# Kernel optimization log

Hardware: AMD Instinct MI355X
Metric: run time of the kernel (lower is better)

Reference implementation:

```python
import jax, jax.numpy as jnp
import numpy as np

N_AGENTS, RNN_H, N_HEADS, GAT_D, EMB, SDIM = 16, 64, 4, 32, 32, 128


def setup_inputs() -> dict:
    key = jax.random.key(0)
    ks = jax.random.split(key, 16)
    xav = lambda k, shp: jax.random.normal(k, shp, jnp.float32) * (2.0 / sum(shp)) ** 0.5
    return {
        'agent_qs': jax.random.normal(ks[0], (32, 128, N_AGENTS), jnp.float32),
        'states': jax.random.normal(ks[1], (32, 128, SDIM), jnp.float32),
        'hidden_states': jax.random.normal(ks[2], (32, 128, N_AGENTS, RNN_H), jnp.float32),
        'uncertainty': jax.random.uniform(ks[3], (32, 128, 1), jnp.float32),
        'W_gat': xav(ks[4], (RNN_H, N_HEADS * GAT_D)) * 1.414,
        'att_a': xav(ks[5], (1, N_HEADS, 2 * GAT_D)) * 1.414,
        'w1s_W': xav(ks[6], (SDIM + 1, N_HEADS * EMB * GAT_D)),
        'w1s_b': jnp.zeros((N_HEADS * EMB * GAT_D,), jnp.float32),
        'b1_W': xav(ks[7], (SDIM, EMB)),
        'b1_b': jnp.zeros((EMB,), jnp.float32),
        'wf_W': xav(ks[8], (SDIM, EMB)),
        'wf_b': jnp.zeros((EMB,), jnp.float32),
        'V1_W': xav(ks[9], (SDIM, EMB)),
        'V1_b': jnp.zeros((EMB,), jnp.float32),
        'V2_W': xav(ks[10], (EMB, 1)),
        'V2_b': jnp.zeros((1,), jnp.float32),
    }


def gat(h, W_gat, att_a):
    B, n, _ = h.shape
    hp = (h @ W_gat).reshape(B, n, N_HEADS, GAT_D).transpose(0, 2, 1, 3)  # (B,H,n,d)
    a_src, a_dst = att_a[0, :, :GAT_D], att_a[0, :, GAT_D:]  # (H,d) each
    # e[b,h,i,j] = <hp_i, a_src> + <hp_j, a_dst>  (same math as concat+dot)
    src = jnp.einsum('bhnd,hd->bhn', hp, a_src)
    dst = jnp.einsum('bhnd,hd->bhn', hp, a_dst)
    e = jax.nn.leaky_relu(src[:, :, :, None] + dst[:, :, None, :], 0.2)
    attn = jax.nn.softmax(e, axis=-1)
    return jax.nn.elu(jnp.einsum('bhij,bhjd->bhid', attn, hp))  # (B,H,n,d)


def reference(agent_qs, states, hidden_states, uncertainty, W_gat, att_a,
              w1s_W, w1s_b, b1_W, b1_b, wf_W, wf_b, V1_W, V1_b, V2_W, V2_b):
    bs = agent_qs.shape[0]
    s = states.reshape(-1, SDIM)                      # (B,S)
    qs = agent_qs.reshape(-1, 1, N_AGENTS)            # (B,1,n)
    hs = hidden_states.reshape(-1, N_AGENTS, RNN_H)   # (B,n,R)
    unc = uncertainty.reshape(-1, 1)
    s_aug = jnp.concatenate([s, unc], axis=1)         # (B,S+1)

    g = gat(hs, W_gat, att_a)                         # (B,H,n,d)

    w1_state = (s_aug @ w1s_W + w1s_b).reshape(-1, N_HEADS, EMB, GAT_D)
    w1_heads = jnp.abs(jnp.einsum('bhed,bhnd->bhen', w1_state, g))  # (B,H,E,n)
    w1 = w1_heads.mean(axis=1).transpose(0, 2, 1)     # (B,n,E)

    b1 = (s @ b1_W + b1_b)[:, None, :]                # (B,1,E)
    hidden = jax.nn.elu(jnp.einsum('bin,bne->bie', qs, w1) + b1)  # (B,1,E)

    w_final = jnp.abs(s @ wf_W + wf_b)[:, :, None]    # (B,E,1)
    v = (jax.nn.relu(s @ V1_W + V1_b) @ V2_W + V2_b)[:, None, :]  # (B,1,1)
    y = jnp.einsum('bie,bej->bij', hidden, w_final) + v
    return y.reshape(bs, -1, 1)
```

## Files before the change

### kernel.cpp

```cpp
#include <hip/hip_runtime.h>
#include <math.h>


typedef __attribute__((ext_vector_type(8))) short short8;
typedef __attribute__((ext_vector_type(8))) unsigned short ushort8;
typedef __attribute__((ext_vector_type(4))) unsigned short ushort4v;
typedef __attribute__((ext_vector_type(4))) float float4v;
typedef __attribute__((ext_vector_type(4))) _Float16 half4v;

static __device__ inline unsigned short f2bf(float f) {
    unsigned int x;
    __builtin_memcpy(&x, &f, 4);
    unsigned int r = x + 0x7fffu + ((x >> 16) & 1u);
    return (unsigned short)(r >> 16);
}

static __device__ inline short8 pack8(float4 f0, float4 f1) {
    ushort8 o;
    o[0] = f2bf(f0.x); o[1] = f2bf(f0.y); o[2] = f2bf(f0.z); o[3] = f2bf(f0.w);
    o[4] = f2bf(f1.x); o[5] = f2bf(f1.y); o[6] = f2bf(f1.z); o[7] = f2bf(f1.w);
    short8 s;
    __builtin_memcpy(&s, &o, 16);
    return s;
}

__global__ __launch_bounds__(256) void k0_prep(
    const float* __restrict__ w1s_W,
    const float* __restrict__ W_gat,
    const float* __restrict__ att_a,
    const float* __restrict__ states,
    const float* __restrict__ b1_W, const float* __restrict__ b1_b,
    const float* __restrict__ wf_W, const float* __restrict__ wf_b,
    const float* __restrict__ V1_W, const float* __restrict__ V1_b,
    const float* __restrict__ V2_W, const float* __restrict__ V2_b,
    unsigned short* __restrict__ w1sTf,
    unsigned short* __restrict__ WgTf,
    float* __restrict__ b1v, float* __restrict__ wfv,
    float* __restrict__ out)
{
    __shared__ __align__(16) char SMEM[49152];
    const int tid = threadIdx.x, bx = blockIdx.x;

    if (bx < 256) {
        unsigned short* T = (unsigned short*)SMEM;
        const int c0 = bx * 16;
        const int cc = tid & 15, kr = tid >> 4;
        #pragma unroll
        for (int t = 0; t < 8; ++t) {
            int k = t * 16 + kr;
            T[cc * 136 + k] = f2bf(w1s_W[(size_t)k * 4096 + c0 + cc]);
        }
        __syncthreads();
        const int ks = tid >> 6, q = (tid >> 4) & 3, mm = tid & 15;
        *(ushort8*)&w1sTf[(size_t)bx * 2048 + tid * 8] =
            *(const ushort8*)&T[mm * 136 + ks * 32 + q * 8];
    } else if (bx == 256) {
        unsigned short* T = (unsigned short*)SMEM;
        #pragma unroll
        for (int t = 0; t < 32; ++t) {
            int i = t * 256 + tid;
            int k = i >> 7, c = i & 127;
            T[c * 72 + k] = f2bf(W_gat[k * 128 + c]);
        }
        __syncthreads();
        #pragma unroll
        for (int t = 0; t < 4; ++t) {
            int i = t * 256 + tid;
            int nt = i >> 7, w = i & 127;
            int kh = w >> 6, q = (w >> 4) & 3, mm = w & 15;
            *(ushort8*)&WgTf[nt * 1024 + w * 8] =
                *(const ushort8*)&T[(nt * 16 + mm) * 72 + kh * 32 + q * 8];
        }
        {
            const int k = tid >> 2, h = tid & 3;
            float ss = 0.f, dd = 0.f;
            #pragma unroll
            for (int d = 0; d < 32; ++d) {
                float wv = W_gat[k * 128 + h * 32 + d];
                ss = fmaf(wv, att_a[h * 64 + d], ss);
                dd = fmaf(wv, att_a[h * 64 + 32 + d], dd);
            }
            const int base = 8192 + (k >> 5) * 512 + ((k >> 3) & 3) * 128 + (k & 7);
            WgTf[base + h * 8]       = f2bf(ss);
            WgTf[base + (4 + h) * 8] = f2bf(dd);
        }
        #pragma unroll
        for (int t = 0; t < 2; ++t) {
            int i = t * 256 + tid;
            int kh = i >> 8, q = (i >> 6) & 3, mm = 8 + ((i >> 3) & 7), j = i & 7;
            WgTf[8192 + kh * 512 + q * 128 + mm * 8 + j] = 0;
        }
    } else {
        float* WL = (float*)SMEM;
        for (int i = tid; i < 12288; i += 256)
            WL[i] = (i < 4096) ? b1_W[i] : (i < 8192 ? wf_W[i - 4096] : V1_W[i - 8192]);
        __syncthreads();

        const int wave = tid >> 6, lane = tid & 63, mm = lane & 15, q = lane >> 4;
        const int b0w = (bx - 257) * 64 + wave * 16;

        short8 a[4];
        #pragma unroll
        for (int ks = 0; ks < 4; ++ks) {
            const float* sp = states + (size_t)(b0w + mm) * 128 + ks * 32 + q * 8;
            a[ks] = pack8(*(const float4*)sp, *(const float4*)(sp + 4));
        }
        float4v accT[6];
        #pragma unroll
        for (int nt = 0; nt < 6; ++nt) accT[nt] = (float4v){0.f, 0.f, 0.f, 0.f};
        #pragma unroll
        for (int nt = 0; nt < 6; ++nt) {
            const int set = nt >> 1, e = (nt & 1) * 16 + mm;
            #pragma unroll
            for (int ks = 0; ks < 4; ++ks) {
                ushort8 bfu;
                #pragma unroll
                for (int j = 0; j < 8; ++j)
                    bfu[j] = f2bf(WL[set * 4096 + (ks * 32 + q * 8 + j) * 32 + e]);
                short8 bf;
                __builtin_memcpy(&bf, &bfu, 16);
                accT[nt] = __builtin_amdgcn_mfma_f32_16x16x32_bf16(a[ks], bf, accT[nt], 0, 0, 0);
            }
        }
        float vsum[4] = {0.f, 0.f, 0.f, 0.f};
        #pragma unroll
        for (int p = 0; p < 2; ++p) {
            const int e = p * 16 + mm;
            const float bb1 = b1_b[e], bwf = wf_b[e], bv1 = V1_b[e], v2 = V2_W[e];
            #pragma unroll
            for (int reg = 0; reg < 4; ++reg) {
                const int row = b0w + q * 4 + reg;
                b1v[(size_t)row * 32 + e] = accT[p][reg] + bb1;
                wfv[(size_t)row * 32 + e] = fabsf(accT[2 + p][reg] + bwf);
                vsum[reg] += fmaxf(accT[4 + p][reg] + bv1, 0.f) * v2;
            }
        }
        #pragma unroll
        for (int reg = 0; reg < 4; ++reg) {
            vsum[reg] += __shfl_xor(vsum[reg], 1);
            vsum[reg] += __shfl_xor(vsum[reg], 2);
            vsum[reg] += __shfl_xor(vsum[reg], 4);
            vsum[reg] += __shfl_xor(vsum[reg], 8);
        }
        if (mm == 0) {
            #pragma unroll
            for (int reg = 0; reg < 4; ++reg)
                out[b0w + q * 4 + reg] = vsum[reg] + V2_b[0];
        }
    }
}

__global__ __launch_bounds__(256) void k1_gat(
    const float* __restrict__ hidden_states,
    const unsigned short* __restrict__ WgTf,
    unsigned short* __restrict__ g_bf)
{
    const int wave = threadIdx.x >> 6;
    const int b = blockIdx.x * 4 + wave;
    const int lane = threadIdx.x & 63, m = lane & 15, quad = lane >> 4;
    __shared__ __align__(16) float sc[4 * 320];
    float* scr = &sc[wave * 320];

    const float* hrow = hidden_states + ((size_t)b * 16 + m) * 64;
    float4 f0 = *(const float4*)(hrow + quad * 8);
    float4 f1 = *(const float4*)(hrow + quad * 8 + 4);
    short8 a0 = pack8(f0, f1);
    f0 = *(const float4*)(hrow + 32 + quad * 8);
    f1 = *(const float4*)(hrow + 32 + quad * 8 + 4);
    short8 a1 = pack8(f0, f1);

    float4v hpt[9];
    #pragma unroll
    for (int nt = 0; nt < 9; ++nt) {
        short8 bf0 = *(const short8*)&WgTf[nt * 1024 + lane * 8];
        short8 bf1 = *(const short8*)&WgTf[nt * 1024 + 512 + lane * 8];
        float4v z = (float4v){0.f, 0.f, 0.f, 0.f};
        z = __builtin_amdgcn_mfma_f32_16x16x32_bf16(a0, bf0, z, 0, 0, 0);
        z = __builtin_amdgcn_mfma_f32_16x16x32_bf16(a1, bf1, z, 0, 0, 0);
        hpt[nt] = z;
    }

    {
        float4 pr = {hpt[8][0], hpt[8][1], hpt[8][2], hpt[8][3]};
        *(float4*)&scr[m * 20 + quad * 4] = pr;
    }

    #pragma unroll
    for (int h = 0; h < 4; ++h) {
        const float src_m = scr[h * 20 + m];
        float4 pdv = *(const float4*)&scr[(4 + h) * 20 + quad * 4];
        float pd[4] = {pdv.x, pdv.y, pdv.z, pdv.w};

        float e_[4];
        #pragma unroll
        for (int jj = 0; jj < 4; ++jj) {
            float x = src_m + pd[jj];
            e_[jj] = fmaxf(x, 0.2f * x);
        }
        float mx = fmaxf(fmaxf(e_[0], e_[1]), fmaxf(e_[2], e_[3]));
        mx = fmaxf(mx, __shfl_xor(mx, 16));
        mx = fmaxf(mx, __shfl_xor(mx, 32));
        float p_[4], ssum = 0.f;
        #pragma unroll
        for (int jj = 0; jj < 4; ++jj) { p_[jj] = __expf(e_[jj] - mx); ssum += p_[jj]; }
        ssum += __shfl_xor(ssum, 16);
        ssum += __shfl_xor(ssum, 32);
        const float inv = __builtin_amdgcn_rcpf(ssum);

        half4v bfrag;
        #pragma unroll
        for (int jj = 0; jj < 4; ++jj) bfrag[jj] = (_Float16)(p_[jj] * inv);

        #pragma unroll
        for (int p = 0; p < 2; ++p) {
            float4v ct = hpt[2 * h + p];
            half4v afrag;
            #pragma unroll
            for (int t = 0; t < 4; ++t) afrag[t] = (_Float16)ct[t];
            float4v z = (float4v){0.f, 0.f, 0.f, 0.f};
            z = __builtin_amdgcn_mfma_f32_16x16x16f16(afrag, bfrag, z, 0, 0, 0);
            ushort4v o;
            #pragma unroll
            for (int t = 0; t < 4; ++t) {
                float x = z[t];
                float ex = __expf(x) - 1.f;
                x = (x > 0.f) ? x : ex;
                o[t] = f2bf(x);
            }
            *(ushort4v*)&g_bf[((size_t)b * 4 + h) * 512 + m * 32 + p * 16 + quad * 4] = o;
        }
    }
}

__global__ __launch_bounds__(256) void k2_mix(
    const float* __restrict__ states,
    const unsigned short* __restrict__ w1sTf,
    const unsigned short* __restrict__ g_bf,
    const float* __restrict__ agent_qs,
    const float* __restrict__ uncertainty,
    const float* __restrict__ w1s_W,
    const float* __restrict__ w1s_b,
    const float* __restrict__ b1v, const float* __restrict__ wfv,
    float* __restrict__ out)
{
    const int r0 = blockIdx.x * 16;
    const int eg = blockIdx.y;
    const int wave = threadIdx.x >> 6;
    const int lane = threadIdx.x & 63, m = lane & 15, quad = lane >> 4;
    __shared__ __align__(16) unsigned short Wt[2][16 * 328];

    short8 a[4];
    #pragma unroll
    for (int ks = 0; ks < 4; ++ks) {
        const float* sp = states + (size_t)(r0 + m) * 128 + ks * 32 + quad * 8;
        a[ks] = pack8(*(const float4*)sp, *(const float4*)(sp + 4));
    }
    float us[4];
    #pragma unroll
    for (int reg = 0; reg < 4; ++reg)
        us[reg] = uncertainty[r0 + quad * 4 + reg];
    float qs_r[4];
    #pragma unroll
    for (int rr = 0; rr < 4; ++rr)
        qs_r[rr] = agent_qs[(r0 + wave * 4 + rr) * 16 + m];

    const float* w128 = w1s_W + (size_t)128 * 4096;
    float Sacc[4][4] = {};

    #pragma unroll
    for (int h = 0; h < 4; ++h) {
        unsigned short* buf = &Wt[h & 1][0];

        #pragma unroll
        for (int t = 0; t < 4; ++t) {
            const int ctl = wave * 4 + t;
            const int ct = h * 64 + eg * 16 + ctl;
            const int c_loc = ctl * 16 + m;
            const int cg = h * 1024 + eg * 256 + c_loc;
            const float wfix = w128[cg], bias = w1s_b[cg];
            float4v acc = (float4v){0.f, 0.f, 0.f, 0.f};
            #pragma unroll
            for (int ks = 0; ks < 4; ++ks) {
                short8 bfr = *(const short8*)&w1sTf[(size_t)ct * 2048 + ks * 512 + lane * 8];
                acc = __builtin_amdgcn_mfma_f32_16x16x32_bf16(a[ks], bfr, acc, 0, 0, 0);
            }
            const int el = c_loc >> 5, d = c_loc & 31;
            #pragma unroll
            for (int reg = 0; reg < 4; ++reg)
                buf[(quad * 4 + reg) * 328 + el * 40 + d] =
                    f2bf(acc[reg] + us[reg] * wfix + bias);
        }

        short8 gf[4];
        #pragma unroll
        for (int rr = 0; rr < 4; ++rr)
            gf[rr] = *(const short8*)&g_bf[((size_t)(r0 + wave * 4 + rr) * 4 + h) * 512 + m * 32 + quad * 8];

        __syncthreads();

        #pragma unroll
        for (int rr = 0; rr < 4; ++rr) {
            const int r = wave * 4 + rr;
            short8 af = *(const short8*)&buf[r * 328 + (m & 7) * 40 + quad * 8];
            float4v z = (float4v){0.f, 0.f, 0.f, 0.f};
            z = __builtin_amdgcn_mfma_f32_16x16x32_bf16(af, gf[rr], z, 0, 0, 0);
            #pragma unroll
            for (int reg = 0; reg < 4; ++reg)
                Sacc[rr][reg] += fabsf(z[reg]);
        }
    }

    #pragma unroll
    for (int rr = 0; rr < 4; ++rr) {
        const int r = r0 + wave * 4 + rr;
        float sn[4];
        #pragma unroll
        for (int reg = 0; reg < 4; ++reg) sn[reg] = Sacc[rr][reg] * qs_r[rr];
        #pragma unroll
        for (int mask = 1; mask <= 8; mask <<= 1) {
            #pragma unroll
            for (int reg = 0; reg < 4; ++reg) sn[reg] += __shfl_xor(sn[reg], mask);
        }
        const float* bb = &b1v[(size_t)r * 32 + eg * 8 + (quad & 1) * 4];
        const float* ww = &wfv[(size_t)r * 32 + eg * 8 + (quad & 1) * 4];
        float4 b4 = *(const float4*)bb;
        float4 w4 = *(const float4*)ww;
        float bq[4] = {b4.x, b4.y, b4.z, b4.w};
        float wq[4] = {w4.x, w4.y, w4.z, w4.w};
        float local = 0.f;
        #pragma unroll
        for (int reg = 0; reg < 4; ++reg) {
            float hid = 0.25f * sn[reg] + bq[reg];
            hid = (hid > 0.f) ? hid : expm1f(hid);
            local = fmaf(hid, wq[reg], local);
        }
        local += __shfl_xor(local, 16);
        if (lane == 0) atomicAdd(&out[r], local);
    }
}

extern "C" void kernel_launch(void* const* d_in, const int* in_sizes, int n_in,
                              void* d_out, int out_size, void* d_ws, size_t ws_size,
                              hipStream_t stream)
{
    const float* agent_qs      = (const float*)d_in[0];
    const float* states        = (const float*)d_in[1];
    const float* hidden_states = (const float*)d_in[2];
    const float* uncertainty   = (const float*)d_in[3];
    const float* W_gat         = (const float*)d_in[4];
    const float* att_a         = (const float*)d_in[5];
    const float* w1s_W         = (const float*)d_in[6];
    const float* w1s_b         = (const float*)d_in[7];
    const float* b1_W          = (const float*)d_in[8];
    const float* b1_b          = (const float*)d_in[9];
    const float* wf_W          = (const float*)d_in[10];
    const float* wf_b          = (const float*)d_in[11];
    const float* V1_W          = (const float*)d_in[12];
    const float* V1_b          = (const float*)d_in[13];
    const float* V2_W          = (const float*)d_in[14];
    const float* V2_b          = (const float*)d_in[15];

    char* w = (char*)d_ws;
    unsigned short* w1sTf   = (unsigned short*)w;  w += (size_t)524288 * 2;
    unsigned short* WgTf    = (unsigned short*)w;  w += (size_t)9216 * 2;
    unsigned short* g_bf    = (unsigned short*)w;  w += (size_t)8388608 * 2;
    float* b1v              = (float*)w;           w += (size_t)131072 * 4;
    float* wfv              = (float*)w;           w += (size_t)131072 * 4;
    float* out              = (float*)d_out;

    k0_prep<<<321, 256, 0, stream>>>(w1s_W, W_gat, att_a, states,
                                     b1_W, b1_b, wf_W, wf_b, V1_W, V1_b,
                                     V2_W, V2_b, w1sTf, WgTf, b1v, wfv, out);

    k1_gat<<<1024, 256, 0, stream>>>(hidden_states, WgTf, g_bf);

    dim3 gmix(256, 4);
    k2_mix<<<gmix, 256, 0, stream>>>(states, w1sTf, g_bf, agent_qs, uncertainty,
                                     w1s_W, w1s_b, b1v, wfv, out);
}
```

Baseline: 136.5 us.

## Fuse prep and GAT kernels, recompute W_gat fragments per block in LDS

Merges the prep kernel and the GAT kernel into a single launch. Each GAT block now rebuilds the bf16 W_gat tile and the folded attention projection in shared memory, so the workspace WgTf buffer and the dependency between the two launches go away. The small state-projection path now converts its weights to bf16 once into a padded LDS layout, so the MFMA loop no longer converts on every read. The cost is redundant W_gat conversion and attention-dot work in each of 1024 GAT blocks, plus a larger shared-memory footprint per block.

New measurement: 140.9 us. 3.2% more time.

```diff
diff --git a/kernel.cpp b/kernel.cpp
--- a/kernel.cpp
+++ b/kernel.cpp
@@ -24,21 +24,22 @@
     return s;
 }
 
-__global__ __launch_bounds__(256) void k0_prep(
+__global__ __launch_bounds__(256) void ka_fused(
     const float* __restrict__ w1s_W,
     const float* __restrict__ W_gat,
     const float* __restrict__ att_a,
     const float* __restrict__ states,
+    const float* __restrict__ hidden_states,
     const float* __restrict__ b1_W, const float* __restrict__ b1_b,
     const float* __restrict__ wf_W, const float* __restrict__ wf_b,
     const float* __restrict__ V1_W, const float* __restrict__ V1_b,
     const float* __restrict__ V2_W, const float* __restrict__ V2_b,
     unsigned short* __restrict__ w1sTf,
-    unsigned short* __restrict__ WgTf,
+    unsigned short* __restrict__ g_bf,
     float* __restrict__ b1v, float* __restrict__ wfv,
     float* __restrict__ out)
 {
-    __shared__ __align__(16) char SMEM[49152];
+    __shared__ __align__(16) char SMEM[26112];
     const int tid = threadIdx.x, bx = blockIdx.x;
 
     if (bx < 256) {
@@ -54,50 +55,17 @@
         const int ks = tid >> 6, q = (tid >> 4) & 3, mm = tid & 15;
         *(ushort8*)&w1sTf[(size_t)bx * 2048 + tid * 8] =
             *(const ushort8*)&T[mm * 136 + ks * 32 + q * 8];
-    } else if (bx == 256) {
-        unsigned short* T = (unsigned short*)SMEM;
-        #pragma unroll
-        for (int t = 0; t < 32; ++t) {
-            int i = t * 256 + tid;
-            int k = i >> 7, c = i & 127;
-            T[c * 72 + k] = f2bf(W_gat[k * 128 + c]);
+    } else if (bx < 320) {
+        unsigned short* WLu = (unsigned short*)SMEM;
+        for (int i = tid; i < 12288; i += 256) {
+            float v = (i < 4096) ? b1_W[i] : (i < 8192 ? wf_W[i - 4096] : V1_W[i - 8192]);
+            int set = i >> 12, k = (i >> 5) & 127, e = i & 31;
+            WLu[set * 4352 + k * 34 + e] = f2bf(v);
         }
         __syncthreads();
-        #pragma unroll
-        for (int t = 0; t < 4; ++t) {
-            int i = t * 256 + tid;
-            int nt = i >> 7, w = i & 127;
-            int kh = w >> 6, q = (w >> 4) & 3, mm = w & 15;
-            *(ushort8*)&WgTf[nt * 1024 + w * 8] =
-                *(const ushort8*)&T[(nt * 16 + mm) * 72 + kh * 32 + q * 8];
-        }
-        {
-            const int k = tid >> 2, h = tid & 3;
-            float ss = 0.f, dd = 0.f;
-            #pragma unroll
-            for (int d = 0; d < 32; ++d) {
-                float wv = W_gat[k * 128 + h * 32 + d];
-                ss = fmaf(wv, att_a[h * 64 + d], ss);
-                dd = fmaf(wv, att_a[h * 64 + 32 + d], dd);
-            }
-            const int base = 8192 + (k >> 5) * 512 + ((k >> 3) & 3) * 128 + (k & 7);
-            WgTf[base + h * 8]       = f2bf(ss);
-            WgTf[base + (4 + h) * 8] = f2bf(dd);
-        }
-        #pragma unroll
-        for (int t = 0; t < 2; ++t) {
-            int i = t * 256 + tid;
-            int kh = i >> 8, q = (i >> 6) & 3, mm = 8 + ((i >> 3) & 7), j = i & 7;
-            WgTf[8192 + kh * 512 + q * 128 + mm * 8 + j] = 0;
-        }
-    } else {
-        float* WL = (float*)SMEM;
-        for (int i = tid; i < 12288; i += 256)
-            WL[i] = (i < 4096) ? b1_W[i] : (i < 8192 ? wf_W[i - 4096] : V1_W[i - 8192]);
-        __syncthreads();
 
         const int wave = tid >> 6, lane = tid & 63, mm = lane & 15, q = lane >> 4;
-        const int b0w = (bx - 257) * 64 + wave * 16;
+        const int b0w = (bx - 256) * 64 + wave * 16;
 
         short8 a[4];
         #pragma unroll
@@ -116,7 +84,7 @@
                 ushort8 bfu;
                 #pragma unroll
                 for (int j = 0; j < 8; ++j)
-                    bfu[j] = f2bf(WL[set * 4096 + (ks * 32 + q * 8 + j) * 32 + e]);
+                    bfu[j] = WLu[set * 4352 + (ks * 32 + q * 8 + j) * 34 + e];
                 short8 bf;
                 __builtin_memcpy(&bf, &bfu, 16);
                 accT[nt] = __builtin_amdgcn_mfma_f32_16x16x32_bf16(a[ks], bf, accT[nt], 0, 0, 0);
@@ -147,87 +115,119 @@
             for (int reg = 0; reg < 4; ++reg)
                 out[b0w + q * 4 + reg] = vsum[reg] + V2_b[0];
         }
-    }
-}
-
-__global__ __launch_bounds__(256) void k1_gat(
-    const float* __restrict__ hidden_states,
-    const unsigned short* __restrict__ WgTf,
-    unsigned short* __restrict__ g_bf)
-{
-    const int wave = threadIdx.x >> 6;
-    const int b = blockIdx.x * 4 + wave;
-    const int lane = threadIdx.x & 63, m = lane & 15, quad = lane >> 4;
-    __shared__ __align__(16) float sc[4 * 320];
-    float* scr = &sc[wave * 320];
-
-    const float* hrow = hidden_states + ((size_t)b * 16 + m) * 64;
-    float4 f0 = *(const float4*)(hrow + quad * 8);
-    float4 f1 = *(const float4*)(hrow + quad * 8 + 4);
-    short8 a0 = pack8(f0, f1);
-    f0 = *(const float4*)(hrow + 32 + quad * 8);
-    f1 = *(const float4*)(hrow + 32 + quad * 8 + 4);
-    short8 a1 = pack8(f0, f1);
-
-    float4v hpt[9];
-    #pragma unroll
-    for (int nt = 0; nt < 9; ++nt) {
-        short8 bf0 = *(const short8*)&WgTf[nt * 1024 + lane * 8];
-        short8 bf1 = *(const short8*)&WgTf[nt * 1024 + 512 + lane * 8];
-        float4v z = (float4v){0.f, 0.f, 0.f, 0.f};
-        z = __builtin_amdgcn_mfma_f32_16x16x32_bf16(a0, bf0, z, 0, 0, 0);
-        z = __builtin_amdgcn_mfma_f32_16x16x32_bf16(a1, bf1, z, 0, 0, 0);
-        hpt[nt] = z;
-    }
-
-    {
-        float4 pr = {hpt[8][0], hpt[8][1], hpt[8][2], hpt[8][3]};
-        *(float4*)&scr[m * 20 + quad * 4] = pr;
-    }
-
-    #pragma unroll
-    for (int h = 0; h < 4; ++h) {
-        const float src_m = scr[h * 20 + m];
-        float4 pdv = *(const float4*)&scr[(4 + h) * 20 + quad * 4];
-        float pd[4] = {pdv.x, pdv.y, pdv.z, pdv.w};
-
-        float e_[4];
-        #pragma unroll
-        for (int jj = 0; jj < 4; ++jj) {
-            float x = src_m + pd[jj];
-            e_[jj] = fmaxf(x, 0.2f * x);
-        }
-        float mx = fmaxf(fmaxf(e_[0], e_[1]), fmaxf(e_[2], e_[3]));
-        mx = fmaxf(mx, __shfl_xor(mx, 16));
-        mx = fmaxf(mx, __shfl_xor(mx, 32));
-        float p_[4], ssum = 0.f;
-        #pragma unroll
-        for (int jj = 0; jj < 4; ++jj) { p_[jj] = __expf(e_[jj] - mx); ssum += p_[jj]; }
-        ssum += __shfl_xor(ssum, 16);
-        ssum += __shfl_xor(ssum, 32);
-        const float inv = __builtin_amdgcn_rcpf(ssum);
-
-        half4v bfrag;
-        #pragma unroll
-        for (int jj = 0; jj < 4; ++jj) bfrag[jj] = (_Float16)(p_[jj] * inv);
-
-        #pragma unroll
-        for (int p = 0; p < 2; ++p) {
-            float4v ct = hpt[2 * h + p];
-            half4v afrag;
-            #pragma unroll
-            for (int t = 0; t < 4; ++t) afrag[t] = (_Float16)ct[t];
+    } else {
+        unsigned short* T = (unsigned short*)SMEM;
+        unsigned short* P = (unsigned short*)(SMEM + 18432);
+        float* sc = (float*)(SMEM + 20480);
+
+        #pragma unroll
+        for (int t = 0; t < 32; ++t) {
+            int i = t * 256 + tid;
+            int k = i >> 7, c = i & 127;
+            T[c * 72 + k] = f2bf(W_gat[k * 128 + c]);
+        }
+        {
+            const int k = tid >> 2, h = tid & 3;
+            float ss = 0.f, dd = 0.f;
+            #pragma unroll
+            for (int d = 0; d < 32; ++d) {
+                float wv = W_gat[k * 128 + h * 32 + d];
+                ss = fmaf(wv, att_a[h * 64 + d], ss);
+                dd = fmaf(wv, att_a[h * 64 + 32 + d], dd);
+            }
+            const int base = (k >> 5) * 512 + ((k >> 3) & 3) * 128 + (k & 7);
+            P[base + h * 8]       = f2bf(ss);
+            P[base + (4 + h) * 8] = f2bf(dd);
+        }
+        #pragma unroll
+        for (int t = 0; t < 2; ++t) {
+            int i = t * 256 + tid;
+            int kh = i >> 8, q2 = (i >> 6) & 3, mm2 = 8 + ((i >> 3) & 7), j = i & 7;
+            P[kh * 512 + q2 * 128 + mm2 * 8 + j] = 0;
+        }
+        __syncthreads();
+
+        const int wave = tid >> 6;
+        const int b = (bx - 320) * 4 + wave;
+        const int lane = tid & 63, m = lane & 15, quad = lane >> 4;
+        float* scr = &sc[wave * 320];
+
+        const float* hrow = hidden_states + ((size_t)b * 16 + m) * 64;
+        float4 f0 = *(const float4*)(hrow + quad * 8);
+        float4 f1 = *(const float4*)(hrow + quad * 8 + 4);
+        short8 a0 = pack8(f0, f1);
+        f0 = *(const float4*)(hrow + 32 + quad * 8);
+        f1 = *(const float4*)(hrow + 32 + quad * 8 + 4);
+        short8 a1 = pack8(f0, f1);
+
+        float4v hpt[9];
+        #pragma unroll
+        for (int nt = 0; nt < 8; ++nt) {
+            short8 bf0 = *(const short8*)&T[(nt * 16 + m) * 72 + quad * 8];
+            short8 bf1 = *(const short8*)&T[(nt * 16 + m) * 72 + 32 + quad * 8];
             float4v z = (float4v){0.f, 0.f, 0.f, 0.f};
-            z = __builtin_amdgcn_mfma_f32_16x16x16f16(afrag, bfrag, z, 0, 0, 0);
-            ushort4v o;
-            #pragma unroll
-            for (int t = 0; t < 4; ++t) {
-                float x = z[t];
-                float ex = __expf(x) - 1.f;
-                x = (x > 0.f) ? x : ex;
-                o[t] = f2bf(x);
-            }
-            *(ushort4v*)&g_bf[((size_t)b * 4 + h) * 512 + m * 32 + p * 16 + quad * 4] = o;
+            z = __builtin_amdgcn_mfma_f32_16x16x32_bf16(a0, bf0, z, 0, 0, 0);
+            z = __builtin_amdgcn_mfma_f32_16x16x32_bf16(a1, bf1, z, 0, 0, 0);
+            hpt[nt] = z;
+        }
+        {
+            short8 bf0 = *(const short8*)&P[lane * 8];
+            short8 bf1 = *(const short8*)&P[512 + lane * 8];
+            float4v z = (float4v){0.f, 0.f, 0.f, 0.f};
+            z = __builtin_amdgcn_mfma_f32_16x16x32_bf16(a0, bf0, z, 0, 0, 0);
+            z = __builtin_amdgcn_mfma_f32_16x16x32_bf16(a1, bf1, z, 0, 0, 0);
+            hpt[8] = z;
+        }
+
+        {
+            float4 pr = {hpt[8][0], hpt[8][1], hpt[8][2], hpt[8][3]};
+            *(float4*)&scr[m * 20 + quad * 4] = pr;
+        }
+
+        #pragma unroll
+        for (int h = 0; h < 4; ++h) {
+            const float src_m = scr[h * 20 + m];
+            float4 pdv = *(const float4*)&scr[(4 + h) * 20 + quad * 4];
+            float pd[4] = {pdv.x, pdv.y, pdv.z, pdv.w};
+
+            float e_[4];
+            #pragma unroll
+            for (int jj = 0; jj < 4; ++jj) {
+                float x = src_m + pd[jj];
+                e_[jj] = fmaxf(x, 0.2f * x);
+            }
+            float mx = fmaxf(fmaxf(e_[0], e_[1]), fmaxf(e_[2], e_[3]));
+            mx = fmaxf(mx, __shfl_xor(mx, 16));
+            mx = fmaxf(mx, __shfl_xor(mx, 32));
+            float p_[4], ssum = 0.f;
+            #pragma unroll
+            for (int jj = 0; jj < 4; ++jj) { p_[jj] = __expf(e_[jj] - mx); ssum += p_[jj]; }
+            ssum += __shfl_xor(ssum, 16);
+            ssum += __shfl_xor(ssum, 32);
+            const float inv = __builtin_amdgcn_rcpf(ssum);
+
+            half4v bfrag;
+            #pragma unroll
+            for (int jj = 0; jj < 4; ++jj) bfrag[jj] = (_Float16)(p_[jj] * inv);
+
+            #pragma unroll
+            for (int p = 0; p < 2; ++p) {
+                float4v ct = hpt[2 * h + p];
+                half4v afrag;
+                #pragma unroll
+                for (int t = 0; t < 4; ++t) afrag[t] = (_Float16)ct[t];
+                float4v z = (float4v){0.f, 0.f, 0.f, 0.f};
+                z = __builtin_amdgcn_mfma_f32_16x16x16f16(afrag, bfrag, z, 0, 0, 0);
+                ushort4v o;
+                #pragma unroll
+                for (int t = 0; t < 4; ++t) {
+                    float x = z[t];
+                    float ex = __expf(x) - 1.f;
+                    x = (x > 0.f) ? x : ex;
+                    o[t] = f2bf(x);
+                }
+                *(ushort4v*)&g_bf[((size_t)b * 4 + h) * 512 + m * 32 + p * 16 + quad * 4] = o;
+            }
         }
     }
 }
@@ -362,17 +362,14 @@
 
     char* w = (char*)d_ws;
     unsigned short* w1sTf   = (unsigned short*)w;  w += (size_t)524288 * 2;
-    unsigned short* WgTf    = (unsigned short*)w;  w += (size_t)9216 * 2;
     unsigned short* g_bf    = (unsigned short*)w;  w += (size_t)8388608 * 2;
     float* b1v              = (float*)w;           w += (size_t)131072 * 4;
     float* wfv              = (float*)w;           w += (size_t)131072 * 4;
     float* out              = (float*)d_out;
 
-    k0_prep<<<321, 256, 0, stream>>>(w1s_W, W_gat, att_a, states,
-                                     b1_W, b1_b, wf_W, wf_b, V1_W, V1_b,
-                                     V2_W, V2_b, w1sTf, WgTf, b1v, wfv, out);
-
-    k1_gat<<<1024, 256, 0, stream>>>(hidden_states, WgTf, g_bf);
+    ka_fused<<<1344, 256, 0, stream>>>(w1s_W, W_gat, att_a, states, hidden_states,
+                                       b1_W, b1_b, wf_W, wf_b, V1_W, V1_b,
+                                       V2_W, V2_b, w1sTf, g_bf, b1v, wfv, out);
 
     dim3 gmix(256, 4);
     k2_mix<<<gmix, 256, 0, stream>>>(states, w1sTf, g_bf, agent_qs, uncertainty,
```
